# Optimization experiments

Hardware: AMD Instinct MI355X
Metric: run time of the kernel (lower is better)

Reference implementation:

```python
import jax, jax.numpy as jnp
import numpy as np

N_NODES = 100000
N_EDGES = 640000
D = 128


def setup_inputs() -> dict:
    key = jax.random.key(0)
    k1, k2, k3 = jax.random.split(key, 3)
    x = jax.random.normal(k1, (N_NODES, D), dtype=jnp.float32)
    W = jax.random.normal(k2, (D, D), dtype=jnp.float32) * (1.0 / np.sqrt(D))
    edge_index = jax.random.randint(k3, (2, N_EDGES), 0, N_NODES, dtype=jnp.int64)
    return {"x": x, "W": W, "edge_index": edge_index}


def reference(x, W, edge_index):
    # Linear (bias-free): x @ W^T matches torch.nn.Linear semantics
    h = jnp.matmul(x, W.T)  # [N, D]
    src, dst = edge_index[0], edge_index[1]
    # message = norm * x_j with norm == 1, aggr='add':
    # out[i] = sum_{(j->i) in E} h[j]
    out = jax.ops.segment_sum(h[src], dst, num_segments=x.shape[0])
    return out
```

## Files before the change

### kernel.cpp

```cpp
#include <hip/hip_runtime.h>
#include <hip/hip_bf16.h>

#define NNODES 100000
#define NEDGES 640000
#define DIM    128
#define CAP    32
#define NCHUNK (NNODES * DIM / 8)

typedef __attribute__((ext_vector_type(8))) __bf16 bf16x8;
typedef __attribute__((ext_vector_type(4))) float  f32x4;

__device__ __forceinline__ uint bf16pair(float a, float b) {
    uint ua = __float_as_uint(a), ub = __float_as_uint(b);
    ua = (ua + 0x7FFFu + ((ua >> 16) & 1u)) >> 16;
    ub = (ub + 0x7FFFu + ((ub >> 16) & 1u)) >> 16;
    return (ub << 16) | (ua & 0xFFFFu);
}

__global__ __launch_bounds__(256) void prep_kernel(
    const float* __restrict__ x, const float* __restrict__ W,
    const int* __restrict__ ei,
    int4* __restrict__ xb4, int4* __restrict__ wb4,
    int* __restrict__ cursor, int* __restrict__ csr)
{
    int id = blockIdx.x * 256 + threadIdx.x;
    const float4* p = reinterpret_cast<const float4*>(x) + (size_t)id * 2;
    float4 f0 = p[0], f1 = p[1];
    int4 v = {(int)bf16pair(f0.x, f0.y), (int)bf16pair(f0.z, f0.w),
              (int)bf16pair(f1.x, f1.y), (int)bf16pair(f1.z, f1.w)};
    xb4[id] = v;
    if (id < 2048) {
        const float4* q = reinterpret_cast<const float4*>(W) + (size_t)id * 2;
        float4 g0 = q[0], g1 = q[1];
        int4 wv = {(int)bf16pair(g0.x, g0.y), (int)bf16pair(g0.z, g0.w),
                   (int)bf16pair(g1.x, g1.y), (int)bf16pair(g1.z, g1.w)};
        wb4[id] = wv;
    }
    if (id < NEDGES) {
        int src = ei[id];
        int dst = ei[NEDGES + id];
        int pos = atomicAdd(&cursor[dst], 1);
        if (pos < CAP) csr[dst * CAP + pos] = src;
    }
}

__global__ __launch_bounds__(1024) void fused_gg(
    const int2* __restrict__ xb, const int4* __restrict__ wb,
    const int* __restrict__ cursor, const int* __restrict__ csr,
    float* __restrict__ out)
{
    __shared__ int4 w_lds[128 * 16];
    __shared__ int4 a_lds[32 * 16];
    int tid = threadIdx.x;
    long base = (long)blockIdx.x * 32;

#pragma unroll
    for (int i = 0; i < 2; ++i) {
        int c = i * 1024 + tid;
        int d = c >> 4, k8 = c & 15;
        w_lds[(c & ~15) | (k8 ^ (d & 7))] = wb[c];
    }

    int hw = tid >> 5, lane = tid & 31;
    {
        long node = base + hw;
        int cnt = cursor[node];
        if (cnt > CAP) cnt = CAP;
        const int* lst = csr + node * CAP;
        int s_l = lst[(lane < cnt) ? lane : 0];
        float4 acc = {0.f, 0.f, 0.f, 0.f};
        int cnt4 = (cnt + 3) & ~3;
        for (int j = 0; j < cnt4; j += 4) {
#pragma unroll
            for (int k = 0; k < 4; ++k) {
                int s = __shfl(s_l, j + k, 32);
                float m = (j + k < cnt) ? 1.0f : 0.0f;
                int2 v = xb[(size_t)s * 32 + lane];
                acc.x = fmaf(m, __uint_as_float((uint)v.x << 16), acc.x);
                acc.y = fmaf(m, __uint_as_float((uint)v.x & 0xFFFF0000u), acc.y);
                acc.z = fmaf(m, __uint_as_float((uint)v.y << 16), acc.z);
                acc.w = fmaf(m, __uint_as_float((uint)v.y & 0xFFFF0000u), acc.w);
            }
        }
        int2 pk = {(int)bf16pair(acc.x, acc.y), (int)bf16pair(acc.z, acc.w)};
        reinterpret_cast<int2*>(a_lds)[hw * 32 + (((lane >> 1) ^ (hw & 7)) << 1) + (lane & 1)] = pk;
    }
    __syncthreads();

    int l64 = tid & 63;
    int w   = tid >> 6;
    int rt  = w >> 3, dt = w & 7;
    int rl  = l64 & 15;
    int kg  = l64 >> 4;

    f32x4 acc = {};
#pragma unroll
    for (int kc = 0; kc < 4; ++kc) {
        int arow = rt * 16 + rl;
        int k8 = kc * 4 + kg;
        int4 araw = a_lds[arow * 16 + (k8 ^ (arow & 7))];
        bf16x8 af = *reinterpret_cast<bf16x8*>(&araw);
        int d = dt * 16 + rl;
        int4 braw = w_lds[d * 16 + (k8 ^ (d & 7))];
        bf16x8 bf = *reinterpret_cast<bf16x8*>(&braw);
        acc = __builtin_amdgcn_mfma_f32_16x16x32_bf16(af, bf, acc, 0, 0, 0);
    }
#pragma unroll
    for (int j = 0; j < 4; ++j)
        out[(base + rt * 16 + kg * 4 + j) * DIM + dt * 16 + rl] = acc[j];
}

extern "C" void kernel_launch(void* const* d_in, const int* in_sizes, int n_in,
                              void* d_out, int out_size, void* d_ws, size_t ws_size,
                              hipStream_t stream) {
    const float* x  = (const float*)d_in[0];
    const float* W  = (const float*)d_in[1];
    const int*   ei = (const int*)d_in[2];
    float* out = (float*)d_out;

    int*  cursor = (int*)d_ws;
    int*  csr    = cursor + 100352;
    int4* xb4    = (int4*)(csr + NNODES * CAP);
    int4* wb4    = xb4 + NCHUNK;

    hipMemsetAsync(cursor, 0, (size_t)100352 * sizeof(int), stream);
    prep_kernel<<<NCHUNK / 256, 256, 0, stream>>>(x, W, ei, xb4, wb4, cursor, csr);
    fused_gg<<<NNODES / 32, 1024, 0, stream>>>(
        (const int2*)xb4, wb4, cursor, csr, out);
}
```

Baseline: 171.5 us.

## Process 64 nodes per block with 16-lane int4 gathers and split prep blocks

The prep kernel now gives edge-bucketing and bf16 conversion their own blocks, so the atomics and the conversion run as separate block populations. The fused kernel handles 64 destination nodes per block. Each node is gathered by 16 lanes doing 16-byte loads, with four loads in flight per iteration. Each wave runs two MFMA row tiles that share one W fragment, which halves the W LDS reads per output and amortizes the W staging over more nodes. The cost is fewer blocks, higher register use, and bounds checks for the partial last block.

```diff
diff --git a/kernel.cpp b/kernel.cpp
--- a/kernel.cpp
+++ b/kernel.cpp
@@ -6,6 +6,8 @@
 #define DIM    128
 #define CAP    32
 #define NCHUNK (NNODES * DIM / 8)
+#define EBLK   (NEDGES / 256)
+#define SBLK   (NCHUNK / 256)
 
 typedef __attribute__((ext_vector_type(8))) __bf16 bf16x8;
 typedef __attribute__((ext_vector_type(4))) float  f32x4;
@@ -23,7 +25,16 @@
     int4* __restrict__ xb4, int4* __restrict__ wb4,
     int* __restrict__ cursor, int* __restrict__ csr)
 {
-    int id = blockIdx.x * 256 + threadIdx.x;
+    int b = blockIdx.x;
+    if (b < EBLK) {
+        int e = b * 256 + threadIdx.x;
+        int src = ei[e];
+        int dst = ei[NEDGES + e];
+        int pos = atomicAdd(&cursor[dst], 1);
+        if (pos < CAP) csr[dst * CAP + pos] = src;
+        return;
+    }
+    int id = (b - EBLK) * 256 + threadIdx.x;
     const float4* p = reinterpret_cast<const float4*>(x) + (size_t)id * 2;
     float4 f0 = p[0], f1 = p[1];
     int4 v = {(int)bf16pair(f0.x, f0.y), (int)bf16pair(f0.z, f0.w),
@@ -36,23 +47,17 @@
                    (int)bf16pair(g1.x, g1.y), (int)bf16pair(g1.z, g1.w)};
         wb4[id] = wv;
     }
-    if (id < NEDGES) {
-        int src = ei[id];
-        int dst = ei[NEDGES + id];
-        int pos = atomicAdd(&cursor[dst], 1);
-        if (pos < CAP) csr[dst * CAP + pos] = src;
-    }
 }
 
 __global__ __launch_bounds__(1024) void fused_gg(
-    const int2* __restrict__ xb, const int4* __restrict__ wb,
+    const int4* __restrict__ xb, const int4* __restrict__ wb,
     const int* __restrict__ cursor, const int* __restrict__ csr,
     float* __restrict__ out)
 {
     __shared__ int4 w_lds[128 * 16];
-    __shared__ int4 a_lds[32 * 16];
+    __shared__ int4 a_lds[64 * 16];
     int tid = threadIdx.x;
-    long base = (long)blockIdx.x * 32;
+    long base = (long)blockIdx.x * 64;
 
 #pragma unroll
     for (int i = 0; i < 2; ++i) {
@@ -61,53 +66,77 @@
         w_lds[(c & ~15) | (k8 ^ (d & 7))] = wb[c];
     }
 
-    int hw = tid >> 5, lane = tid & 31;
+    int g = tid >> 4, l = tid & 15;
     {
-        long node = base + hw;
-        int cnt = cursor[node];
+        long node = base + g;
+        int cnt = 0;
+        if (node < NNODES) cnt = cursor[node];
         if (cnt > CAP) cnt = CAP;
         const int* lst = csr + node * CAP;
-        int s_l = lst[(lane < cnt) ? lane : 0];
-        float4 acc = {0.f, 0.f, 0.f, 0.f};
+        int2 sp = reinterpret_cast<const int2*>(lst)[l];
+        int safe = __shfl(sp.x, 0, 16);
+        sp.x = (2 * l     < cnt) ? sp.x : safe;
+        sp.y = (2 * l + 1 < cnt) ? sp.y : safe;
+        float4 accA = {0.f, 0.f, 0.f, 0.f}, accB = {0.f, 0.f, 0.f, 0.f};
         int cnt4 = (cnt + 3) & ~3;
         for (int j = 0; j < cnt4; j += 4) {
-#pragma unroll
-            for (int k = 0; k < 4; ++k) {
-                int s = __shfl(s_l, j + k, 32);
-                float m = (j + k < cnt) ? 1.0f : 0.0f;
-                int2 v = xb[(size_t)s * 32 + lane];
-                acc.x = fmaf(m, __uint_as_float((uint)v.x << 16), acc.x);
-                acc.y = fmaf(m, __uint_as_float((uint)v.x & 0xFFFF0000u), acc.y);
-                acc.z = fmaf(m, __uint_as_float((uint)v.y << 16), acc.z);
-                acc.w = fmaf(m, __uint_as_float((uint)v.y & 0xFFFF0000u), acc.w);
-            }
+            int h = j >> 1;
+            int s0 = __shfl(sp.x, h, 16),     s1 = __shfl(sp.y, h, 16);
+            int s2 = __shfl(sp.x, h + 1, 16), s3 = __shfl(sp.y, h + 1, 16);
+            int4 v0 = xb[(size_t)s0 * 16 + l];
+            int4 v1 = xb[(size_t)s1 * 16 + l];
+            int4 v2 = xb[(size_t)s2 * 16 + l];
+            int4 v3 = xb[(size_t)s3 * 16 + l];
+            float m0 = (j     < cnt) ? 1.f : 0.f, m1 = (j + 1 < cnt) ? 1.f : 0.f;
+            float m2 = (j + 2 < cnt) ? 1.f : 0.f, m3 = (j + 3 < cnt) ? 1.f : 0.f;
+#define ACC(vv, mm)                                                        \
+            accA.x = fmaf(mm, __uint_as_float((uint)(vv).x << 16), accA.x);       \
+            accA.y = fmaf(mm, __uint_as_float((uint)(vv).x & 0xFFFF0000u), accA.y);\
+            accA.z = fmaf(mm, __uint_as_float((uint)(vv).y << 16), accA.z);       \
+            accA.w = fmaf(mm, __uint_as_float((uint)(vv).y & 0xFFFF0000u), accA.w);\
+            accB.x = fmaf(mm, __uint_as_float((uint)(vv).z << 16), accB.x);       \
+            accB.y = fmaf(mm, __uint_as_float((uint)(vv).z & 0xFFFF0000u), accB.y);\
+            accB.z = fmaf(mm, __uint_as_float((uint)(vv).w << 16), accB.z);       \
+            accB.w = fmaf(mm, __uint_as_float((uint)(vv).w & 0xFFFF0000u), accB.w);
+            ACC(v0, m0) ACC(v1, m1) ACC(v2, m2) ACC(v3, m3)
+#undef ACC
         }
-        int2 pk = {(int)bf16pair(acc.x, acc.y), (int)bf16pair(acc.z, acc.w)};
-        reinterpret_cast<int2*>(a_lds)[hw * 32 + (((lane >> 1) ^ (hw & 7)) << 1) + (lane & 1)] = pk;
+        int4 pk = {(int)bf16pair(accA.x, accA.y), (int)bf16pair(accA.z, accA.w),
+                   (int)bf16pair(accB.x, accB.y), (int)bf16pair(accB.z, accB.w)};
+        a_lds[g * 16 + (l ^ (g & 7))] = pk;
     }
     __syncthreads();
 
     int l64 = tid & 63;
     int w   = tid >> 6;
-    int rt  = w >> 3, dt = w & 7;
+    int dt  = w & 7;
+    int rt0 = (w >> 3) * 2;
     int rl  = l64 & 15;
     int kg  = l64 >> 4;
 
-    f32x4 acc = {};
+    f32x4 acc0 = {}, acc1 = {};
 #pragma unroll
     for (int kc = 0; kc < 4; ++kc) {
-        int arow = rt * 16 + rl;
         int k8 = kc * 4 + kg;
-        int4 araw = a_lds[arow * 16 + (k8 ^ (arow & 7))];
-        bf16x8 af = *reinterpret_cast<bf16x8*>(&araw);
         int d = dt * 16 + rl;
         int4 braw = w_lds[d * 16 + (k8 ^ (d & 7))];
         bf16x8 bf = *reinterpret_cast<bf16x8*>(&braw);
-        acc = __builtin_amdgcn_mfma_f32_16x16x32_bf16(af, bf, acc, 0, 0, 0);
+        int a0r = rt0 * 16 + rl;
+        int4 a0raw = a_lds[a0r * 16 + (k8 ^ (a0r & 7))];
+        bf16x8 af0 = *reinterpret_cast<bf16x8*>(&a0raw);
+        acc0 = __builtin_amdgcn_mfma_f32_16x16x32_bf16(af0, bf, acc0, 0, 0, 0);
+        int a1r = (rt0 + 1) * 16 + rl;
+        int4 a1raw = a_lds[a1r * 16 + (k8 ^ (a1r & 7))];
+        bf16x8 af1 = *reinterpret_cast<bf16x8*>(&a1raw);
+        acc1 = __builtin_amdgcn_mfma_f32_16x16x32_bf16(af1, bf, acc1, 0, 0, 0);
     }
 #pragma unroll
-    for (int j = 0; j < 4; ++j)
-        out[(base + rt * 16 + kg * 4 + j) * DIM + dt * 16 + rl] = acc[j];
+    for (int j = 0; j < 4; ++j) {
+        long r0 = base + rt0 * 16 + kg * 4 + j;
+        if (r0 < NNODES) out[r0 * DIM + dt * 16 + rl] = acc0[j];
+        long r1 = base + (rt0 + 1) * 16 + kg * 4 + j;
+        if (r1 < NNODES) out[r1 * DIM + dt * 16 + rl] = acc1[j];
+    }
 }
 
 extern "C" void kernel_launch(void* const* d_in, const int* in_sizes, int n_in,
@@ -124,7 +153,7 @@
     int4* wb4    = xb4 + NCHUNK;
 
     hipMemsetAsync(cursor, 0, (size_t)100352 * sizeof(int), stream);
-    prep_kernel<<<NCHUNK / 256, 256, 0, stream>>>(x, W, ei, xb4, wb4, cursor, csr);
-    fused_gg<<<NNODES / 32, 1024, 0, stream>>>(
-        (const int2*)xb4, wb4, cursor, csr, out);
+    prep_kernel<<<EBLK + SBLK, 256, 0, stream>>>(x, W, ei, xb4, wb4, cursor, csr);
+    fused_gg<<<(NNODES + 63) / 64, 1024, 0, stream>>>(
+        xb4, wb4, cursor, csr, out);
 }
```

After: 164.5 us. 1.04x faster.
